# Kernel optimization log

Hardware: AMD Instinct MI355X
Metric: run time of the kernel (lower is better)

## Reference

```python
import jax, jax.numpy as jnp
import numpy as np

N, D = 10000, 20
NODE_DIM = 172
D_T = 172
EDGE_DIM = 172
N_HEAD = 2
D_MODEL = NODE_DIM + EDGE_DIM + D_T  # 516


def _layer_norm(x, g, b, eps=1e-5):
    mu = jnp.mean(x, axis=-1, keepdims=True)
    var = jnp.mean((x - mu) ** 2, axis=-1, keepdims=True)
    return (x - mu) / jnp.sqrt(var + eps) * g + b


def setup_inputs() -> dict:
    key = jax.random.key(0)
    ks = jax.random.split(key, 12)
    d_k = D_MODEL // N_HEAD
    std_qk = np.sqrt(2.0 / (D_MODEL + d_k)).astype(np.float32)
    node_h = jax.random.normal(ks[0], (N, NODE_DIM), jnp.float32)
    edge_t = jax.random.uniform(ks[1], (N, D), jnp.float32, 0.0, 100.0)
    edge_feat = jax.random.normal(ks[2], (N, D, EDGE_DIM), jnp.float32)
    nbr_idx = jax.random.randint(ks[3], (N, D), 0, N)
    t_now = jnp.array([100.0], jnp.float32)
    # weights stored [in, out]; apply as x @ W
    w_q = jax.random.normal(ks[4], (D_MODEL, N_HEAD * d_k), jnp.float32) * std_qk
    w_k = jax.random.normal(ks[5], (D_MODEL, N_HEAD * d_k), jnp.float32) * std_qk
    w_v = jax.random.normal(ks[6], (D_MODEL, N_HEAD * d_k), jnp.float32) * std_qk
    basis_freq = jnp.asarray(1.0 / 10 ** np.linspace(0, 9, D_T), jnp.float32)
    phase = jnp.zeros((D_T,), jnp.float32)
    ln_gamma = jnp.ones((D_MODEL,), jnp.float32)
    ln_beta = jnp.zeros((D_MODEL,), jnp.float32)
    fc_w = jax.random.normal(ks[7], (N_HEAD * d_k, D_MODEL), jnp.float32) * np.float32(np.sqrt(2.0 / (N_HEAD * d_k + D_MODEL)))
    fc_b = jnp.zeros((D_MODEL,), jnp.float32)
    m1_w = jax.random.normal(ks[8], (D_MODEL + NODE_DIM, NODE_DIM), jnp.float32) * np.float32(np.sqrt(2.0 / (D_MODEL + 2 * NODE_DIM)))
    m1_b = jnp.zeros((NODE_DIM,), jnp.float32)
    m2_w = jax.random.normal(ks[9], (NODE_DIM, NODE_DIM), jnp.float32) * np.float32(np.sqrt(1.0 / NODE_DIM))
    m2_b = jnp.zeros((NODE_DIM,), jnp.float32)
    return dict(node_h=node_h, edge_t=edge_t, edge_feat=edge_feat, nbr_idx=nbr_idx,
                t_now=t_now, n_head=N_HEAD, w_q=w_q, w_k=w_k, w_v=w_v,
                basis_freq=basis_freq, phase=phase, ln_gamma=ln_gamma, ln_beta=ln_beta,
                fc_w=fc_w, fc_b=fc_b, m1_w=m1_w, m1_b=m1_b, m2_w=m2_w, m2_b=m2_b)


def reference(node_h, edge_t, edge_feat, nbr_idx, t_now, n_head, w_q, w_k, w_v,
              basis_freq, phase, ln_gamma, ln_beta, fc_w, fc_b, m1_w, m1_b, m2_w, m2_b):
    n, deg = edge_t.shape
    d_model = w_q.shape[0]
    d_t = basis_freq.shape[0]
    edge_dim = d_model - node_h.shape[1] - d_t
    d_k = d_model // n_head
    # message_func: per-edge cosine time encoding + k/v projections
    t_enc = jnp.cos((t_now[0] - edge_t)[..., None] * basis_freq + phase)  # [N,D,d_T]
    z = jnp.concatenate([node_h[nbr_idx], edge_feat, t_enc], axis=-1)     # [N,D,d_model]
    k = z @ w_k                                                            # [N,D,H*dk]
    v = z @ w_v
    # reduce_func: self query (zero edge feat, cos(phase) time enc)
    self_z = jnp.concatenate([node_h,
                              jnp.zeros((n, edge_dim), node_h.dtype),
                              jnp.ones((n, d_t), node_h.dtype) * jnp.cos(phase)], axis=-1)
    q = self_z @ w_q                                                       # [N,H*dk]
    # reproduce the exact torch permute/view sequence (head-major flatten)
    qh = q.reshape(n, 1, n_head, d_k).transpose(2, 0, 1, 3).reshape(-1, 1, d_model)
    kh = k.reshape(n, deg, n_head, d_k).transpose(2, 0, 1, 3).reshape(-1, deg, d_model)
    vh = v.reshape(n, deg, n_head, d_k).transpose(2, 0, 1, 3).reshape(-1, deg, d_model)
    attn = jnp.einsum('bqd,bkd->bqk', qh, kh) / jnp.asarray(d_k ** 0.5, qh.dtype)
    attn = jax.nn.softmax(attn, axis=2)
    out = jnp.einsum('bqk,bkd->bqd', attn, vh)                             # [N,1,d_model]
    out = out[:, 0, :].reshape(n_head, n, d_k).transpose(1, 0, 2).reshape(n, -1)
    out = out @ fc_w + fc_b                                                # attn_fc (dropout in eval)
    h = _layer_norm(out + self_z, ln_gamma, ln_beta)
    # merger MLP
    x = jnp.concatenate([h, node_h], axis=-1)
    return jax.nn.relu(x @ m1_w + m1_b) @ m2_w + m2_b
```

## Files before the change

kernel.cpp:

```cpp
#include <hip/hip_runtime.h>
#include <hip/hip_bf16.h>
#include <math.h>

typedef __bf16 bf16;
typedef __attribute__((ext_vector_type(4))) __bf16 bf16x4;
typedef __attribute__((ext_vector_type(8))) __bf16 bf16x8;
typedef __attribute__((ext_vector_type(4))) float f32x4;

constexpr int NN   = 10000;
constexpr int NPAD = 10112;
constexpr int BM = 128, BN = 176, BK = 64;

constexpr size_t FCWT_OFF = 0;
constexpr size_t M1WT_OFF = 608256;
constexpr size_t M2WT_OFF = 856064;
constexpr size_t WKH_OFF  = 923648;
constexpr size_t WQHT_OFF = 1660928;
constexpr size_t WVH_OFF  = 2111488;
constexpr size_t WQKT_OFF = 3012608;
constexpr size_t WVFT_OFF = 3485696;
constexpr size_t QB_OFF   = 4702208;
constexpr size_t QKB_OFF  = 4706304;
constexpr size_t CPH_OFF  = 4714496;
constexpr size_t NH16_OFF = 4715520;
constexpr size_t QK_OFF   = NH16_OFF + (size_t)NPAD*192*2;
constexpr size_t ZB_OFF   = QK_OFF   + (size_t)NPAD*1152*2;
constexpr size_t FCR_OFF  = ZB_OFF   + (size_t)NPAD*1152*2;
constexpr size_t X_OFF    = FCR_OFF  + (size_t)NN*516*4;

typedef __attribute__((address_space(3))) void lds_void;
typedef const __attribute__((address_space(1))) void glb_void;
__device__ __forceinline__ void gload16(const void* g, void* l) {
    __builtin_amdgcn_global_load_lds((glb_void*)(uintptr_t)g,
                                     (lds_void*)(unsigned int)(uintptr_t)l, 16, 0, 0);
}

__global__ __launch_bounds__(256)
void packT_kernel(const float* __restrict__ fcw, const float* __restrict__ m1w,
                  const float* __restrict__ m2w,
                  bf16* __restrict__ FCWT, bf16* __restrict__ M1WT, bf16* __restrict__ M2WT) {
    __shared__ float tile[32][33];
    const float* src; bf16* dst; int K, C, LD;
    switch (blockIdx.y) {
        case 0:  src = fcw; K = 516; C = 516; dst = FCWT; LD = 576; break;
        case 1:  src = m1w; K = 688; C = 172; dst = M1WT; LD = 704; break;
        default: src = m2w; K = 172; C = 172; dst = M2WT; LD = 192; break;
    }
    const int tilesC = (C + 31) >> 5, tilesK = (K + 31) >> 5;
    const int nt = tilesC * tilesK;
    const int tx = threadIdx.x & 31, ty = threadIdx.x >> 5;
    for (int tb = blockIdx.x; tb < nt; tb += gridDim.x) {
        int tc = tb % tilesC, tk = tb / tilesC;
        #pragma unroll
        for (int i = 0; i < 4; ++i) {
            int k = tk*32 + ty + i*8, c = tc*32 + tx;
            tile[ty + i*8][tx] = (k < K && c < C) ? src[(size_t)k*C + c] : 0.f;
        }
        __syncthreads();
        #pragma unroll
        for (int i = 0; i < 4; ++i) {
            int c = tc*32 + ty + i*8, k = tk*32 + tx;
            if (c < C && k < K) dst[(size_t)c*LD + k] = (bf16)tile[tx][ty + i*8];
        }
        __syncthreads();
    }
}

__global__ void pack_misc_kernel(const float* __restrict__ wk, const float* __restrict__ wq,
                                 const float* __restrict__ wv, const float* __restrict__ node_h,
                                 const float* __restrict__ phase,
                                 bf16* __restrict__ WKH, bf16* __restrict__ WQHT,
                                 bf16* __restrict__ WVH, bf16* __restrict__ nh16,
                                 float* __restrict__ cph) {
    constexpr int T0 = 2*516*258;
    constexpr int T1 = T0 + 2*172*258;
    constexpr int T2 = T1 + 2*516*258;
    constexpr int T3 = T2 + NN*192;
    constexpr int T4 = T3 + 172;
    for (int idx = blockIdx.x * blockDim.x + threadIdx.x; idx < T4;
         idx += gridDim.x * blockDim.x) {
        if (idx < T0) {
            int h = idx / (516*258), rem = idx % (516*258), d = rem / 258, j = rem % 258;
            WKH[((size_t)h*576 + d)*320 + j] = (bf16)wk[(size_t)d*516 + h*258 + j];
        } else if (idx < T1) {
            int i = idx - T0;
            int h = i / (172*258), rem = i % (172*258), k = rem / 258, j = rem % 258;
            WQHT[((size_t)h*352 + k)*320 + j] = (bf16)wq[(size_t)k*516 + h*258 + j];
        } else if (idx < T2) {
            int i = idx - T1;
            int h = i / (516*258), rem = i % (516*258), c = rem / 258, j = rem % 258;
            WVH[((size_t)h*704 + c)*320 + j] = (bf16)wv[(size_t)c*516 + h*258 + j];
        } else if (idx < T3) {
            int i = idx - T2, r = i / 192, c = i % 192;
            nh16[i] = (c < 172) ? (bf16)node_h[(size_t)r*172 + c] : (bf16)0.f;
        } else cph[idx - T3] = cosf(phase[idx - T3]);
    }
}

__global__ __launch_bounds__(256)
void qbias_kernel(const float* __restrict__ w_q, const float* __restrict__ phase,
                  float* __restrict__ q_bias) {
    __shared__ float red[256];
    const int c = blockIdx.x, j = threadIdx.x;
    red[j] = (j < 172) ? cosf(phase[j]) * w_q[(size_t)(344 + j) * 516 + c] : 0.f;
    __syncthreads();
    #pragma unroll
    for (int o = 128; o; o >>= 1) { if (j < o) red[j] += red[j + o]; __syncthreads(); }
    if (j == 0) q_bias[c] = red[0];
}

__global__ __launch_bounds__(256)
void qkb_kernel(const float* __restrict__ wk, const float* __restrict__ QB,
                float* __restrict__ qkb) {
    __shared__ float red[256];
    const int hd = blockIdx.x, h = hd / 576, d = hd % 576, t = threadIdx.x;
    float a = 0.f;
    if (d < 516) {
        a = QB[h*258 + t] * wk[(size_t)d*516 + h*258 + t];
        if (t < 2) a += QB[h*258 + 256 + t] * wk[(size_t)d*516 + h*258 + 256 + t];
    }
    red[t] = a; __syncthreads();
    #pragma unroll
    for (int o = 128; o; o >>= 1) { if (t < o) red[t] += red[t + o]; __syncthreads(); }
    if (t == 0) qkb[hd] = red[0];
}

template<int KP, int EPI>
__global__ __launch_bounds__(256, 2)
void gemm_kernel(const bf16* __restrict__ A, int lda, const bf16* __restrict__ Bt,
                 float* __restrict__ outF, bf16* __restrict__ outB, int ldo,
                 const float* __restrict__ bias,
                 const float* __restrict__ aux0, const float* __restrict__ aux1,
                 int Mreal, int Nreal) {
    constexpr int NT = KP / BK;
    __shared__ __align__(16) bf16 As[2][BM][BK];
    __shared__ __align__(16) bf16 Bs[2][BN][BK];

    const int tid  = threadIdx.x;
    const int w    = tid >> 6;
    const int lane = tid & 63;
    const int lr   = lane & 15;
    const int ls   = lane >> 4;
    const int lrow = lane >> 3;
    const int lcol = (lane & 7) * 8;

    const bf16* aBase = A  + (size_t)(blockIdx.y * BM + w * 32 + lrow) * lda + lcol;
    const bf16* bBase = Bt + (size_t)(blockIdx.x * BN + lrow) * KP + lcol;

    auto stage = [&](int buf, int k0) {
        #pragma unroll
        for (int i = 0; i < 4; ++i)
            gload16(aBase + (size_t)(i * 8) * lda + k0, &As[buf][w * 32 + i * 8][0]);
        #pragma unroll
        for (int jj = 0; jj < 6; ++jj) {
            int j = jj * 4 + w;
            if (j < 22) gload16(bBase + (size_t)(j * 8) * KP + k0, &Bs[buf][j * 8][0]);
        }
    };

    f32x4 acc[2][11];
    #pragma unroll
    for (int a = 0; a < 2; ++a)
        #pragma unroll
        for (int b2 = 0; b2 < 11; ++b2) acc[a][b2] = (f32x4)(0.0f);

    stage(0, 0);
    __syncthreads();
    int cur = 0;
    for (int t = 0; t < NT; ++t) {
        if (t + 1 < NT) stage(cur ^ 1, (t + 1) * BK);
        #pragma unroll
        for (int kk = 0; kk < 2; ++kk) {
            bf16x8 a0 = *(const bf16x8*)&As[cur][w*32 +      lr][kk*32 + ls*8];
            bf16x8 a1 = *(const bf16x8*)&As[cur][w*32 + 16 + lr][kk*32 + ls*8];
            #pragma unroll
            for (int nt = 0; nt < 11; ++nt) {
                bf16x8 bfr = *(const bf16x8*)&Bs[cur][nt*16 + lr][kk*32 + ls*8];
                acc[0][nt] = __builtin_amdgcn_mfma_f32_16x16x32_bf16(a0, bfr, acc[0][nt], 0, 0, 0);
                acc[1][nt] = __builtin_amdgcn_mfma_f32_16x16x32_bf16(a1, bfr, acc[1][nt], 0, 0, 0);
            }
        }
        __syncthreads();
        cur ^= 1;
    }

    const int colb = blockIdx.x * BN + lr;
    const int rowb = blockIdx.y * BM + w*32 + ls*4;
    #pragma unroll
    for (int mt = 0; mt < 2; ++mt)
    #pragma unroll
    for (int nt = 0; nt < 11; ++nt)
    #pragma unroll
    for (int q2 = 0; q2 < 4; ++q2) {
        int row = rowb + mt*16 + q2;
        int col = colb + nt*16;
        if (row >= Mreal) continue;
        float v = acc[mt][nt][q2];
        if constexpr (EPI == 0) {
            if (col < Nreal) outB[(size_t)row*ldo + col] = (bf16)(v + bias[col]);
        } else {
            if (col < Nreal) {
                float sz = (col < 172) ? aux0[(size_t)row*172 + col]
                                       : ((col < 344) ? 0.f : aux1[col - 344]);
                outF[(size_t)row*ldo + col] = v + bias[col] + sz;
            }
        }
    }
}

__global__ __launch_bounds__(256, 2)
void gemm_multi_kernel(const bf16* __restrict__ WKH, const bf16* __restrict__ WQHT,
                       const bf16* __restrict__ FCWT, const bf16* __restrict__ WVH,
                       bf16* __restrict__ WQKT, bf16* __restrict__ WVFT) {
    constexpr int KP = 320, NT = KP / BK;
    const int z = blockIdx.z, h = z & 1;
    const bf16 *A, *Bt; bf16* outB; int lda, ldo, Mreal, Nreal;
    if (z < 2) {
        if (blockIdx.x >= 2) return;
        A = WKH + (size_t)h*576*320;  lda = 320;
        Bt = WQHT + (size_t)h*352*320;
        outB = WQKT + (size_t)h*576*192; ldo = 192; Mreal = 576; Nreal = 192;
    } else {
        A = FCWT + (size_t)h*258;     lda = 576;
        Bt = WVH + (size_t)h*704*320;
        outB = WVFT + (size_t)h*576;  ldo = 1152; Mreal = 516; Nreal = 576;
    }
    __shared__ __align__(16) bf16 As[2][BM][BK];
    __shared__ __align__(16) bf16 Bs[2][BN][BK];
    const int tid = threadIdx.x, w = tid >> 6, lane = tid & 63;
    const int lr = lane & 15, ls = lane >> 4;
    const int lrow = lane >> 3, lcol = (lane & 7) * 8;
    const bf16* aBase = A  + (size_t)(blockIdx.y * BM + w * 32 + lrow) * lda + lcol;
    const bf16* bBase = Bt + (size_t)(blockIdx.x * BN + lrow) * KP + lcol;
    auto stage = [&](int buf, int k0) {
        #pragma unroll
        for (int i = 0; i < 4; ++i)
            gload16(aBase + (size_t)(i * 8) * lda + k0, &As[buf][w * 32 + i * 8][0]);
        #pragma unroll
        for (int jj = 0; jj < 6; ++jj) {
            int j = jj * 4 + w;
            if (j < 22) gload16(bBase + (size_t)(j * 8) * KP + k0, &Bs[buf][j * 8][0]);
        }
    };
    f32x4 acc[2][11];
    #pragma unroll
    for (int a = 0; a < 2; ++a)
        #pragma unroll
        for (int b2 = 0; b2 < 11; ++b2) acc[a][b2] = (f32x4)(0.0f);
    stage(0, 0);
    __syncthreads();
    int cur = 0;
    for (int t = 0; t < NT; ++t) {
        if (t + 1 < NT) stage(cur ^ 1, (t + 1) * BK);
        #pragma unroll
        for (int kk = 0; kk < 2; ++kk) {
            bf16x8 a0 = *(const bf16x8*)&As[cur][w*32 +      lr][kk*32 + ls*8];
            bf16x8 a1 = *(const bf16x8*)&As[cur][w*32 + 16 + lr][kk*32 + ls*8];
            #pragma unroll
            for (int nt = 0; nt < 11; ++nt) {
                bf16x8 bfr = *(const bf16x8*)&Bs[cur][nt*16 + lr][kk*32 + ls*8];
                acc[0][nt] = __builtin_amdgcn_mfma_f32_16x16x32_bf16(a0, bfr, acc[0][nt], 0, 0, 0);
                acc[1][nt] = __builtin_amdgcn_mfma_f32_16x16x32_bf16(a1, bfr, acc[1][nt], 0, 0, 0);
            }
        }
        __syncthreads();
        cur ^= 1;
    }
    const int colb = blockIdx.x * BN + lr;
    const int rowb = blockIdx.y * BM + w*32 + ls*4;
    #pragma unroll
    for (int mt = 0; mt < 2; ++mt)
    #pragma unroll
    for (int nt = 0; nt < 11; ++nt)
    #pragma unroll
    for (int q2 = 0; q2 < 4; ++q2) {
        int row = rowb + mt*16 + q2;
        int col = colb + nt*16;
        if (row < Mreal && col < Nreal)
            outB[(size_t)row*ldo + col] = (bf16)acc[mt][nt][q2];
    }
}

__global__ __launch_bounds__(256, 3)
void attn_lite_kernel(const bf16* __restrict__ QK, const bf16* __restrict__ nh16,
                      const float* __restrict__ edge_feat, const float* __restrict__ edge_t,
                      const int* __restrict__ nbr_idx, const float* __restrict__ freq,
                      const float* __restrict__ ph, const float* __restrict__ tnow,
                      bf16* __restrict__ ZB) {
    __shared__ __align__(16) bf16 zs[40 * 576];
    __shared__ __align__(16) float G[40][4];
    __shared__ float sfreq[172], sph[172];
    __shared__ float sdt[40];
    __shared__ int   ssrc[40];
    __shared__ float pp[2][20];

    const int r  = blockIdx.x;
    const int iA = 2 * r;
    const int t  = threadIdx.x;
    const int w  = t >> 6, lane = t & 63;
    const int lr = lane & 15, ls = lane >> 4;

    auto zsa = [&](int row, int c) -> bf16* {
        unsigned b = (unsigned)(row * 1152 + c * 2) ^ (unsigned)((row & 7) << 4);
        return (bf16*)((char*)zs + b);
    };

    f32x4 efA[4], efB[4];
    #pragma unroll
    for (int s = 0; s < 4; ++s) {
        int idx = t + (s + 3) * 256;
        if (idx >= 880 && idx < 1720) {
            int i2 = idx - 880;
            int row = i2 / 21, c = 22 + i2 % 21;
            const float* ep = edge_feat + (size_t)(iA * 20 + row) * 172 + (c * 8 - 172);
            efA[s] = *(const f32x4*)ep;
            efB[s] = *(const f32x4*)(ep + 4);
        }
    }

    if (t < 172) { sfreq[t] = freq[t]; sph[t] = ph[t]; }
    if (t >= 192 && t < 232) {
        int e2 = t - 192, ge = iA * 20 + e2;
        sdt[e2]  = tnow[0] - edge_t[ge];
        ssrc[e2] = nbr_idx[ge];
    }
    __syncthreads();

    #pragma unroll
    for (int it = 0; it < 4; ++it) {
        int idx = t + it * 256;
        if (idx < 880) {
            int row = idx / 22, c = idx % 22;
            bf16x8 v;
            if (c < 21) {
                v = *(const bf16x8*)(nh16 + (size_t)ssrc[row] * 192 + c * 8);
            } else {
                int ge = iA * 20 + row;
                #pragma unroll
                for (int e = 0; e < 8; ++e) {
                    int k = 168 + e;
                    v[e] = (k < 172) ? nh16[(size_t)ssrc[row] * 192 + k]
                                     : (bf16)edge_feat[(size_t)ge * 172 + (k - 172)];
                }
            }
            *(bf16x8*)zsa(row, c * 8) = v;
        }
    }
    #pragma unroll
    for (int it = 6; it < 12; ++it) {
        int idx = t + it * 256;
        if (idx >= 1720 && idx < 2880) {
            int row, c;
            bf16x8 v;
            if (idx < 2600) {
                int i3 = idx - 1720;
                row = i3 / 22; c = 43 + i3 % 22;
                float dt = sdt[row];
                int k0 = c * 8;
                #pragma unroll
                for (int e = 0; e < 8; ++e) {
                    int k = k0 + e;
                    v[e] = (k < 516) ? (bf16)__cosf(dt * sfreq[k - 344] + sph[k - 344]) : (bf16)0.f;
                }
            } else {
                int i4 = idx - 2600;
                row = i4 / 7; c = 65 + i4 % 7;
                #pragma unroll
                for (int e = 0; e < 8; ++e) v[e] = (bf16)0.f;
            }
            *(bf16x8*)zsa(row, c * 8) = v;
        }
    }
    #pragma unroll
    for (int s = 0; s < 4; ++s) {
        int idx = t + (s + 3) * 256;
        if (idx >= 880 && idx < 1720) {
            int i2 = idx - 880;
            int row = i2 / 21, c = 22 + i2 % 21;
            bf16x8 v;
            #pragma unroll
            for (int e = 0; e < 4; ++e) { v[e] = (bf16)efA[s][e]; v[e+4] = (bf16)efB[s][e]; }
            *(bf16x8*)zsa(row, c * 8) = v;
        }
    }
    __syncthreads();

    if (w < 3) {
        int brow = w * 16 + lr; if (brow > 39) brow = 39;
        const bf16* aQK = QK + (size_t)(iA + ((lr >> 1) & 1)) * 1152 + (lane & 1) * 576;
        f32x4 acc = (f32x4)(0.0f);
        __builtin_amdgcn_s_setprio(1);
        #pragma unroll
        for (int ks = 0; ks < 18; ++ks) {
            bf16x8 af = *(const bf16x8*)(aQK + ks * 32 + ls * 8);
            bf16x8 bf = *(const bf16x8*)zsa(brow, ks * 32 + ls * 8);
            acc = __builtin_amdgcn_mfma_f32_16x16x32_bf16(af, bf, acc, 0, 0, 0);
        }
        __builtin_amdgcn_s_setprio(0);
        int col = w * 16 + lr;
        if (ls == 0 && col < 40) *(f32x4*)&G[col][0] = acc;
    }
    __syncthreads();

    if (t < 64) {
        int h = lane >> 5, knbr = lane & 31;
        bool act = knbr < 20;
        float l = -1e30f;
        if (act) {
            int z0 = (knbr / 10) * 20 + 2 * (knbr % 10);
            l = (G[z0][h] + G[z0 + 1][2 + h]) * 0.0622573006f;
        }
        float m = l;
        #pragma unroll
        for (int o = 16; o >= 1; o >>= 1) m = fmaxf(m, __shfl_xor(m, o));
        float e = act ? __expf(l - m) : 0.f;
        float s2 = e;
        #pragma unroll
        for (int o = 16; o >= 1; o >>= 1) s2 += __shfl_xor(s2, o);
        if (act) pp[h][knbr] = e / s2;
    }
    __syncthreads();

    #pragma unroll
    for (int it = 0; it < 2; ++it) {
        int idx = t + it * 256;
        if (idx < 288) {
            int nsel = idx / 144, c4 = (idx % 144) * 4;
            float a0[4] = {0.f, 0.f, 0.f, 0.f};
            float a1[4] = {0.f, 0.f, 0.f, 0.f};
            #pragma unroll
            for (int knbr = 0; knbr < 20; ++knbr) {
                int z0 = (knbr / 10) * 20 + 2 * (knbr % 10) + nsel;
                bf16x4 zv = *(const bf16x4*)zsa(z0, c4);
                float p0 = pp[0][knbr], p1 = pp[1][knbr];
                #pragma unroll
                for (int i = 0; i < 4; ++i) {
                    float zf = (float)zv[i];
                    a0[i] += p0 * zf;
                    a1[i] += p1 * zf;
                }
            }
            bf16x4 o0, o1;
            #pragma unroll
            for (int i = 0; i < 4; ++i) { o0[i] = (bf16)a0[i]; o1[i] = (bf16)a1[i]; }
            *(bf16x4*)(ZB + (size_t)(iA + nsel) * 1152 + c4)       = o0;
            *(bf16x4*)(ZB + (size_t)(iA + nsel) * 1152 + 576 + c4) = o1;
        }
    }
}

__global__ __launch_bounds__(256)
void ln_x_kernel(const float* __restrict__ fcr, const float* __restrict__ g,
                 const float* __restrict__ b, const bf16* __restrict__ nh16,
                 bf16* __restrict__ X) {
    __shared__ float red[2][4];
    __shared__ float mb[2];
    const size_t i = blockIdx.x;
    const int t = threadIdx.x;
    int c0 = t, c1 = t + 256, c2 = t + 512;
    float v0 = fcr[i*516 + c0];
    float v1 = (c1 < 516) ? fcr[i*516 + c1] : 0.f;
    float v2 = (c2 < 516) ? fcr[i*516 + c2] : 0.f;
    float s = v0 + v1 + v2, ss = v0*v0 + v1*v1 + v2*v2;
    #pragma unroll
    for (int o = 32; o; o >>= 1) { s += __shfl_down(s, o); ss += __shfl_down(ss, o); }
    if ((t & 63) == 0) { red[0][t >> 6] = s; red[1][t >> 6] = ss; }
    __syncthreads();
    if (t == 0) {
        float S  = red[0][0] + red[0][1] + red[0][2] + red[0][3];
        float SS = red[1][0] + red[1][1] + red[1][2] + red[1][3];
        float mean = S / 516.f;
        float var  = SS / 516.f - mean*mean;
        mb[0] = mean; mb[1] = rsqrtf(var + 1e-5f);
    }
    __syncthreads();
    float mean = mb[0], rstd = mb[1];
    X[i*704 + c0] = (bf16)((v0 - mean)*rstd*g[c0] + b[c0]);
    if (c1 < 516) X[i*704 + c1] = (bf16)((v1 - mean)*rstd*g[c1] + b[c1]);
    if (c2 < 516) X[i*704 + c2] = (bf16)((v2 - mean)*rstd*g[c2] + b[c2]);
    for (int c = 516 + t; c < 704; c += 256)
        X[i*704 + c] = (c < 688) ? nh16[i*192 + (c - 516)] : (bf16)0.f;
}

__global__ __launch_bounds__(256)
void m1m2_kernel(const bf16* __restrict__ A, const bf16* __restrict__ B1,
                 const bf16* __restrict__ B2, const float* __restrict__ b1,
                 const float* __restrict__ b2, float* __restrict__ outF, int Mreal) {
    constexpr int KP = 704, NT = KP / BK;
    __shared__ __align__(16) union {
        struct { bf16 As[2][BM][BK]; bf16 Bs[2][BN][BK]; } g;
        struct { bf16 Rs[BM][192];  bf16 B2s[BN][192]; } s;
    } U;

    const int tid  = threadIdx.x;
    const int w    = tid >> 6;
    const int lane = tid & 63;
    const int lr   = lane & 15;
    const int ls   = lane >> 4;
    const int lrow = lane >> 3;
    const int lcol = (lane & 7) * 8;

    const bf16* aBase = A  + (size_t)(blockIdx.y * BM + w * 32 + lrow) * KP + lcol;
    const bf16* bBase = B1 + (size_t)lrow * KP + lcol;

    auto stage = [&](int buf, int k0) {
        #pragma unroll
        for (int i = 0; i < 4; ++i)
            gload16(aBase + (size_t)(i * 8) * KP + k0, &U.g.As[buf][w * 32 + i * 8][0]);
        #pragma unroll
        for (int jj = 0; jj < 6; ++jj) {
            int j = jj * 4 + w;
            if (j < 22) gload16(bBase + (size_t)(j * 8) * KP + k0, &U.g.Bs[buf][j * 8][0]);
        }
    };

    f32x4 acc[2][11];
    #pragma unroll
    for (int a = 0; a < 2; ++a)
        #pragma unroll
        for (int b = 0; b < 11; ++b) acc[a][b] = (f32x4)(0.0f);

    stage(0, 0);
    __syncthreads();
    int cur = 0;
    for (int t = 0; t < NT; ++t) {
        if (t + 1 < NT) stage(cur ^ 1, (t + 1) * BK);
        #pragma unroll
        for (int kk = 0; kk < 2; ++kk) {
            bf16x8 a0 = *(const bf16x8*)&U.g.As[cur][w*32 +      lr][kk*32 + ls*8];
            bf16x8 a1 = *(const bf16x8*)&U.g.As[cur][w*32 + 16 + lr][kk*32 + ls*8];
            #pragma unroll
            for (int nt = 0; nt < 11; ++nt) {
                bf16x8 bfr = *(const bf16x8*)&U.g.Bs[cur][nt*16 + lr][kk*32 + ls*8];
                acc[0][nt] = __builtin_amdgcn_mfma_f32_16x16x32_bf16(a0, bfr, acc[0][nt], 0, 0, 0);
                acc[1][nt] = __builtin_amdgcn_mfma_f32_16x16x32_bf16(a1, bfr, acc[1][nt], 0, 0, 0);
            }
        }
        __syncthreads();
        cur ^= 1;
    }

    #pragma unroll
    for (int mt = 0; mt < 2; ++mt)
    #pragma unroll
    for (int nt = 0; nt < 11; ++nt)
    #pragma unroll
    for (int q2 = 0; q2 < 4; ++q2) {
        int lro = w*32 + mt*16 + ls*4 + q2;
        int col = lr + nt*16;
        float vv = (col < 172) ? fmaxf(acc[mt][nt][q2] + b1[col], 0.f) : 0.f;
        U.s.Rs[lro][col] = (bf16)vv;
    }
    for (int idx = tid; idx < BM*16; idx += 256)
        U.s.Rs[idx >> 4][176 + (idx & 15)] = (bf16)0.f;
    #pragma unroll
    for (int jj = 0; jj < 17; ++jj) {
        int j = jj * 4 + w;
        if (j < 66)
            gload16(B2 + (size_t)j*512 + lane*8, (bf16*)U.s.B2s + (size_t)j*512 + lane*8);
    }
    __syncthreads();

    f32x4 acc2[2][11];
    #pragma unroll
    for (int a = 0; a < 2; ++a)
        #pragma unroll
        for (int b = 0; b < 11; ++b) acc2[a][b] = (f32x4)(0.0f);
    #pragma unroll
    for (int t2 = 0; t2 < 3; ++t2) {
        #pragma unroll
        for (int kk = 0; kk < 2; ++kk) {
            int off = t2*64 + kk*32 + ls*8;
            bf16x8 a0 = *(const bf16x8*)&U.s.Rs[w*32 +      lr][off];
            bf16x8 a1 = *(const bf16x8*)&U.s.Rs[w*32 + 16 + lr][off];
            #pragma unroll
            for (int nt = 0; nt < 11; ++nt) {
                bf16x8 bfr = *(const bf16x8*)&U.s.B2s[nt*16 + lr][off];
                acc2[0][nt] = __builtin_amdgcn_mfma_f32_16x16x32_bf16(a0, bfr, acc2[0][nt], 0, 0, 0);
                acc2[1][nt] = __builtin_amdgcn_mfma_f32_16x16x32_bf16(a1, bfr, acc2[1][nt], 0, 0, 0);
            }
        }
    }

    const int rowb = blockIdx.y * BM + w*32 + ls*4;
    #pragma unroll
    for (int mt = 0; mt < 2; ++mt)
    #pragma unroll
    for (int nt = 0; nt < 11; ++nt)
    #pragma unroll
    for (int q2 = 0; q2 < 4; ++q2) {
        int row = rowb + mt*16 + q2;
        int col = lr + nt*16;
        if (row < Mreal && col < 172)
            outF[(size_t)row*172 + col] = acc2[mt][nt][q2] + b2[col];
    }
}

extern "C" void kernel_launch(void* const* d_in, const int* in_sizes, int n_in,
                              void* d_out, int out_size, void* d_ws, size_t ws_size,
                              hipStream_t stream) {
    const float* node_h     = (const float*)d_in[0];
    const float* edge_t     = (const float*)d_in[1];
    const float* edge_feat  = (const float*)d_in[2];
    const int*   nbr_idx    = (const int*)d_in[3];
    const float* t_now      = (const float*)d_in[4];
    const float* w_q        = (const float*)d_in[6];
    const float* w_k        = (const float*)d_in[7];
    const float* w_v        = (const float*)d_in[8];
    const float* basis_freq = (const float*)d_in[9];
    const float* phase      = (const float*)d_in[10];
    const float* ln_g       = (const float*)d_in[11];
    const float* ln_b       = (const float*)d_in[12];
    const float* fc_w       = (const float*)d_in[13];
    const float* fc_b       = (const float*)d_in[14];
    const float* m1_w       = (const float*)d_in[15];
    const float* m1_b       = (const float*)d_in[16];
    const float* m2_w       = (const float*)d_in[17];
    const float* m2_b       = (const float*)d_in[18];

    char* ws = (char*)d_ws;
    bf16*  FCWT = (bf16*)(ws + FCWT_OFF);
    bf16*  M1WT = (bf16*)(ws + M1WT_OFF);
    bf16*  M2WT = (bf16*)(ws + M2WT_OFF);
    bf16*  WKH  = (bf16*)(ws + WKH_OFF);
    bf16*  WQHT = (bf16*)(ws + WQHT_OFF);
    bf16*  WVH  = (bf16*)(ws + WVH_OFF);
    bf16*  WQKT = (bf16*)(ws + WQKT_OFF);
    bf16*  WVFT = (bf16*)(ws + WVFT_OFF);
    float* QB   = (float*)(ws + QB_OFF);
    float* QKB  = (float*)(ws + QKB_OFF);
    float* CPH  = (float*)(ws + CPH_OFF);
    bf16*  NH16 = (bf16*)(ws + NH16_OFF);
    bf16*  QK   = (bf16*)(ws + QK_OFF);
    bf16*  ZB   = (bf16*)(ws + ZB_OFF);
    float* FCR  = (float*)(ws + FCR_OFF);
    bf16*  Xb   = (bf16*)(ws + X_OFF);

    hipMemsetAsync(ws, 0, NH16_OFF, stream);

    packT_kernel<<<dim3(289, 3), 256, 0, stream>>>(fc_w, m1_w, m2_w, FCWT, M1WT, M2WT);
    pack_misc_kernel<<<2048, 256, 0, stream>>>(w_k, w_q, w_v, node_h, phase,
                                               WKH, WQHT, WVH, NH16, CPH);
    qbias_kernel<<<516, 256, 0, stream>>>(w_q, phase, QB);
    qkb_kernel<<<1152, 256, 0, stream>>>(w_k, QB, QKB);

    gemm_multi_kernel<<<dim3(4, 5, 4), 256, 0, stream>>>(WKH, WQHT, FCWT, WVH, WQKT, WVFT);

    gemm_kernel<192, 0><<<dim3(7, 79), 256, 0, stream>>>(
        NH16, 192, WQKT, nullptr, QK, 1152, QKB, nullptr, nullptr, NN, 1152);

    attn_lite_kernel<<<NN / 2, 256, 0, stream>>>(
        QK, NH16, edge_feat, edge_t, nbr_idx, basis_freq, phase, t_now, ZB);

    gemm_kernel<1152, 2><<<dim3(3, 79), 256, 0, stream>>>(
        ZB, 1152, WVFT, FCR, nullptr, 516, fc_b, node_h, CPH, NN, 516);

    ln_x_kernel<<<NN, 256, 0, stream>>>(FCR, ln_g, ln_b, NH16, Xb);

    m1m2_kernel<<<dim3(1, 79), 256, 0, stream>>>(
        Xb, M1WT, M2WT, m1_b, m2_b, (float*)d_out, NN);
}
```

Before: 263.8 us.

## Process two node pairs per attention block with register-staged prefetch overlap

The attention kernel now handles two node pairs per block and launches half as many blocks. While the first pair's scores, softmax and weighted sum are computed, the second pair's gathered neighbor features and edge features are loaded from global memory into registers. The edge-feature boundary chunk is now read with vector loads instead of per-element scalar loads. This aims to hide gather latency behind compute, at the cost of more registers and extra barriers, which may lower occupancy.

```diff
diff --git a/kernel.cpp b/kernel.cpp
--- a/kernel.cpp
+++ b/kernel.cpp
@@ -290,163 +290,185 @@
     __shared__ __align__(16) bf16 zs[40 * 576];
     __shared__ __align__(16) float G[40][4];
     __shared__ float sfreq[172], sph[172];
-    __shared__ float sdt[40];
-    __shared__ int   ssrc[40];
+    __shared__ float sdt[2][40];
+    __shared__ int   ssrc[2][40];
     __shared__ float pp[2][20];
 
-    const int r  = blockIdx.x;
-    const int iA = 2 * r;
-    const int t  = threadIdx.x;
-    const int w  = t >> 6, lane = t & 63;
-    const int lr = lane & 15, ls = lane >> 4;
+    const int t    = threadIdx.x;
+    const int w    = t >> 6, lane = t & 63;
+    const int lr   = lane & 15, ls = lane >> 4;
+    const int rp0  = blockIdx.x * 2;
 
     auto zsa = [&](int row, int c) -> bf16* {
         unsigned b = (unsigned)(row * 1152 + c * 2) ^ (unsigned)((row & 7) << 4);
         return (bf16*)((char*)zs + b);
     };
 
-    f32x4 efA[4], efB[4];
-    #pragma unroll
-    for (int s = 0; s < 4; ++s) {
-        int idx = t + (s + 3) * 256;
-        if (idx >= 880 && idx < 1720) {
-            int i2 = idx - 880;
-            int row = i2 / 21, c = 22 + i2 % 21;
-            const float* ep = edge_feat + (size_t)(iA * 20 + row) * 172 + (c * 8 - 172);
-            efA[s] = *(const f32x4*)ep;
-            efB[s] = *(const f32x4*)(ep + 4);
-        }
-    }
-
     if (t < 172) { sfreq[t] = freq[t]; sph[t] = ph[t]; }
-    if (t >= 192 && t < 232) {
-        int e2 = t - 192, ge = iA * 20 + e2;
-        sdt[e2]  = tnow[0] - edge_t[ge];
-        ssrc[e2] = nbr_idx[ge];
-    }
-    __syncthreads();
-
-    #pragma unroll
-    for (int it = 0; it < 4; ++it) {
-        int idx = t + it * 256;
-        if (idx < 880) {
-            int row = idx / 22, c = idx % 22;
-            bf16x8 v;
-            if (c < 21) {
-                v = *(const bf16x8*)(nh16 + (size_t)ssrc[row] * 192 + c * 8);
-            } else {
-                int ge = iA * 20 + row;
+    if (t >= 176) {
+        int e2 = t - 176;
+        int ge = rp0 * 40 + e2;
+        sdt[e2 / 40][e2 % 40]  = tnow[0] - edge_t[ge];
+        ssrc[e2 / 40][e2 % 40] = nbr_idx[ge];
+    }
+    __syncthreads();
+
+    bf16x8 nhA[4]; bf16x4 nhm[4]; f32x4 efm[4]; f32x4 efA[4], efB[4];
+
+    auto STAGE = [&](int p) {
+        const int base = (rp0 + p) * 40;
+        #pragma unroll
+        for (int s = 0; s < 4; ++s) {
+            int i = t + s * 256;
+            if (i < 880) {
+                int row = i / 22, c = i % 22;
+                if (c < 21) {
+                    nhA[s] = *(const bf16x8*)(nh16 + (size_t)ssrc[p][row] * 192 + c * 8);
+                } else {
+                    nhm[s] = *(const bf16x4*)(nh16 + (size_t)ssrc[p][row] * 192 + 168);
+                    efm[s] = *(const f32x4*)(edge_feat + (size_t)(base + row) * 172);
+                }
+            }
+        }
+        #pragma unroll
+        for (int s = 0; s < 4; ++s) {
+            int i2 = t + s * 256;
+            if (i2 < 840) {
+                int row = i2 / 21, c = 22 + i2 % 21;
+                const float* ep = edge_feat + (size_t)(base + row) * 172 + (c * 8 - 172);
+                efA[s] = *(const f32x4*)ep;
+                efB[s] = *(const f32x4*)(ep + 4);
+            }
+        }
+    };
+
+    auto WRITE = [&](int p) {
+        #pragma unroll
+        for (int s = 0; s < 4; ++s) {
+            int i = t + s * 256;
+            if (i < 880) {
+                int row = i / 22, c = i % 22;
+                if (c < 21) {
+                    *(bf16x8*)zsa(row, c * 8) = nhA[s];
+                } else {
+                    bf16x8 v;
+                    v[0] = nhm[s][0]; v[1] = nhm[s][1]; v[2] = nhm[s][2]; v[3] = nhm[s][3];
+                    v[4] = (bf16)efm[s][0]; v[5] = (bf16)efm[s][1];
+                    v[6] = (bf16)efm[s][2]; v[7] = (bf16)efm[s][3];
+                    *(bf16x8*)zsa(row, 168) = v;
+                }
+            }
+        }
+        #pragma unroll
+        for (int s = 0; s < 4; ++s) {
+            int i2 = t + s * 256;
+            if (i2 < 840) {
+                int row = i2 / 21, c = 22 + i2 % 21;
+                bf16x8 v;
                 #pragma unroll
-                for (int e = 0; e < 8; ++e) {
-                    int k = 168 + e;
-                    v[e] = (k < 172) ? nh16[(size_t)ssrc[row] * 192 + k]
-                                     : (bf16)edge_feat[(size_t)ge * 172 + (k - 172)];
+                for (int e = 0; e < 4; ++e) { v[e] = (bf16)efA[s][e]; v[e+4] = (bf16)efB[s][e]; }
+                *(bf16x8*)zsa(row, c * 8) = v;
+            }
+        }
+        #pragma unroll
+        for (int it = 6; it < 12; ++it) {
+            int idx = t + it * 256;
+            if (idx >= 1720 && idx < 2880) {
+                int row, c; bf16x8 v;
+                if (idx < 2600) {
+                    int i3 = idx - 1720;
+                    row = i3 / 22; c = 43 + i3 % 22;
+                    float dt = sdt[p][row];
+                    int k0 = c * 8;
+                    #pragma unroll
+                    for (int e = 0; e < 8; ++e) {
+                        int k = k0 + e;
+                        v[e] = (k < 516) ? (bf16)__cosf(dt * sfreq[k - 344] + sph[k - 344]) : (bf16)0.f;
+                    }
+                } else {
+                    int i4 = idx - 2600;
+                    row = i4 / 7; c = 65 + i4 % 7;
+                    #pragma unroll
+                    for (int e = 0; e < 8; ++e) v[e] = (bf16)0.f;
                 }
-            }
-            *(bf16x8*)zsa(row, c * 8) = v;
-        }
-    }
-    #pragma unroll
-    for (int it = 6; it < 12; ++it) {
-        int idx = t + it * 256;
-        if (idx >= 1720 && idx < 2880) {
-            int row, c;
-            bf16x8 v;
-            if (idx < 2600) {
-                int i3 = idx - 1720;
-                row = i3 / 22; c = 43 + i3 % 22;
-                float dt = sdt[row];
-                int k0 = c * 8;
+                *(bf16x8*)zsa(row, c * 8) = v;
+            }
+        }
+    };
+
+    auto COMPUTE = [&](int p) {
+        const int iA = (rp0 + p) * 2;
+        if (w < 3) {
+            int brow = w * 16 + lr; if (brow > 39) brow = 39;
+            const bf16* aQK = QK + (size_t)(iA + ((lr >> 1) & 1)) * 1152 + (lane & 1) * 576;
+            f32x4 acc = (f32x4)(0.0f);
+            __builtin_amdgcn_s_setprio(1);
+            #pragma unroll
+            for (int ks = 0; ks < 18; ++ks) {
+                bf16x8 af = *(const bf16x8*)(aQK + ks * 32 + ls * 8);
+                bf16x8 bf = *(const bf16x8*)zsa(brow, ks * 32 + ls * 8);
+                acc = __builtin_amdgcn_mfma_f32_16x16x32_bf16(af, bf, acc, 0, 0, 0);
+            }
+            __builtin_amdgcn_s_setprio(0);
+            int col = w * 16 + lr;
+            if (ls == 0 && col < 40) *(f32x4*)&G[col][0] = acc;
+        }
+        __syncthreads();
+        if (t < 64) {
+            int h = lane >> 5, knbr = lane & 31;
+            bool act = knbr < 20;
+            float l = -1e30f;
+            if (act) {
+                int z0 = (knbr / 10) * 20 + 2 * (knbr % 10);
+                l = (G[z0][h] + G[z0 + 1][2 + h]) * 0.0622573006f;
+            }
+            float m = l;
+            #pragma unroll
+            for (int o = 16; o >= 1; o >>= 1) m = fmaxf(m, __shfl_xor(m, o));
+            float e = act ? __expf(l - m) : 0.f;
+            float s2 = e;
+            #pragma unroll
+            for (int o = 16; o >= 1; o >>= 1) s2 += __shfl_xor(s2, o);
+            if (act) pp[h][knbr] = e / s2;
+        }
+        __syncthreads();
+        #pragma unroll
+        for (int it = 0; it < 2; ++it) {
+            int idx = t + it * 256;
+            if (idx < 288) {
+                int nsel = idx / 144, c4 = (idx % 144) * 4;
+                float a0[4] = {0.f, 0.f, 0.f, 0.f};
+                float a1[4] = {0.f, 0.f, 0.f, 0.f};
                 #pragma unroll
-                for (int e = 0; e < 8; ++e) {
-                    int k = k0 + e;
-                    v[e] = (k < 516) ? (bf16)__cosf(dt * sfreq[k - 344] + sph[k - 344]) : (bf16)0.f;
+                for (int knbr = 0; knbr < 20; ++knbr) {
+                    int z0 = (knbr / 10) * 20 + 2 * (knbr % 10) + nsel;
+                    bf16x4 zv = *(const bf16x4*)zsa(z0, c4);
+                    float p0 = pp[0][knbr], p1 = pp[1][knbr];
+                    #pragma unroll
+                    for (int i = 0; i < 4; ++i) {
+                        float zf = (float)zv[i];
+                        a0[i] += p0 * zf;
+                        a1[i] += p1 * zf;
+                    }
                 }
-            } else {
-                int i4 = idx - 2600;
-                row = i4 / 7; c = 65 + i4 % 7;
+                bf16x4 o0, o1;
                 #pragma unroll
-                for (int e = 0; e < 8; ++e) v[e] = (bf16)0.f;
-            }
-            *(bf16x8*)zsa(row, c * 8) = v;
-        }
-    }
-    #pragma unroll
-    for (int s = 0; s < 4; ++s) {
-        int idx = t + (s + 3) * 256;
-        if (idx >= 880 && idx < 1720) {
-            int i2 = idx - 880;
-            int row = i2 / 21, c = 22 + i2 % 21;
-            bf16x8 v;
-            #pragma unroll
-            for (int e = 0; e < 4; ++e) { v[e] = (bf16)efA[s][e]; v[e+4] = (bf16)efB[s][e]; }
-            *(bf16x8*)zsa(row, c * 8) = v;
-        }
-    }
-    __syncthreads();
-
-    if (w < 3) {
-        int brow = w * 16 + lr; if (brow > 39) brow = 39;
-        const bf16* aQK = QK + (size_t)(iA + ((lr >> 1) & 1)) * 1152 + (lane & 1) * 576;
-        f32x4 acc = (f32x4)(0.0f);
-        __builtin_amdgcn_s_setprio(1);
-        #pragma unroll
-        for (int ks = 0; ks < 18; ++ks) {
-            bf16x8 af = *(const bf16x8*)(aQK + ks * 32 + ls * 8);
-            bf16x8 bf = *(const bf16x8*)zsa(brow, ks * 32 + ls * 8);
-            acc = __builtin_amdgcn_mfma_f32_16x16x32_bf16(af, bf, acc, 0, 0, 0);
-        }
-        __builtin_amdgcn_s_setprio(0);
-        int col = w * 16 + lr;
-        if (ls == 0 && col < 40) *(f32x4*)&G[col][0] = acc;
-    }
-    __syncthreads();
-
-    if (t < 64) {
-        int h = lane >> 5, knbr = lane & 31;
-        bool act = knbr < 20;
-        float l = -1e30f;
-        if (act) {
-            int z0 = (knbr / 10) * 20 + 2 * (knbr % 10);
-            l = (G[z0][h] + G[z0 + 1][2 + h]) * 0.0622573006f;
-        }
-        float m = l;
-        #pragma unroll
-        for (int o = 16; o >= 1; o >>= 1) m = fmaxf(m, __shfl_xor(m, o));
-        float e = act ? __expf(l - m) : 0.f;
-        float s2 = e;
-        #pragma unroll
-        for (int o = 16; o >= 1; o >>= 1) s2 += __shfl_xor(s2, o);
-        if (act) pp[h][knbr] = e / s2;
-    }
-    __syncthreads();
-
-    #pragma unroll
-    for (int it = 0; it < 2; ++it) {
-        int idx = t + it * 256;
-        if (idx < 288) {
-            int nsel = idx / 144, c4 = (idx % 144) * 4;
-            float a0[4] = {0.f, 0.f, 0.f, 0.f};
-            float a1[4] = {0.f, 0.f, 0.f, 0.f};
-            #pragma unroll
-            for (int knbr = 0; knbr < 20; ++knbr) {
-                int z0 = (knbr / 10) * 20 + 2 * (knbr % 10) + nsel;
-                bf16x4 zv = *(const bf16x4*)zsa(z0, c4);
-                float p0 = pp[0][knbr], p1 = pp[1][knbr];
-                #pragma unroll
-                for (int i = 0; i < 4; ++i) {
-                    float zf = (float)zv[i];
-                    a0[i] += p0 * zf;
-                    a1[i] += p1 * zf;
-                }
-            }
-            bf16x4 o0, o1;
-            #pragma unroll
-            for (int i = 0; i < 4; ++i) { o0[i] = (bf16)a0[i]; o1[i] = (bf16)a1[i]; }
-            *(bf16x4*)(ZB + (size_t)(iA + nsel) * 1152 + c4)       = o0;
-            *(bf16x4*)(ZB + (size_t)(iA + nsel) * 1152 + 576 + c4) = o1;
-        }
-    }
+                for (int i = 0; i < 4; ++i) { o0[i] = (bf16)a0[i]; o1[i] = (bf16)a1[i]; }
+                *(bf16x4*)(ZB + (size_t)(iA + nsel) * 1152 + c4)       = o0;
+                *(bf16x4*)(ZB + (size_t)(iA + nsel) * 1152 + 576 + c4) = o1;
+            }
+        }
+    };
+
+    STAGE(0);
+    WRITE(0);
+    __syncthreads();
+    STAGE(1);
+    COMPUTE(0);
+    __syncthreads();
+    WRITE(1);
+    __syncthreads();
+    COMPUTE(1);
 }
 
 __global__ __launch_bounds__(256)
@@ -649,7 +671,7 @@
     gemm_kernel<192, 0><<<dim3(7, 79), 256, 0, stream>>>(
         NH16, 192, WQKT, nullptr, QK, 1152, QKB, nullptr, nullptr, NN, 1152);
 
-    attn_lite_kernel<<<NN / 2, 256, 0, stream>>>(
+    attn_lite_kernel<<<NN / 4, 256, 0, stream>>>(
         QK, NH16, edge_feat, edge_t, nbr_idx, basis_freq, phase, t_now, ZB);
 
     gemm_kernel<1152, 2><<<dim3(3, 79), 256, 0, stream>>>(
```

New measurement: 273.3 us. 3.6% more time.

## Halve GEMM M-tile to 64 rows and split fused m1m2 into two GEMMs

Applied to the files above, without the earlier changes.

Parameterizes the generic GEMM on M-tile size and launches all main GEMMs with 64-row tiles, doubling the grid to fill more CUs on the 10000-row problems. The fused m1/m2 MLP kernel, which ran only 79 blocks, is replaced by two launches of the generic GEMM (ReLU+bf16 epilogue, then bias epilogue) with an intermediate buffer in workspace. This trades extra B-tile reloads per block and an extra global round-trip plus launch for much higher parallelism.

```diff
diff --git a/kernel.cpp b/kernel.cpp
--- a/kernel.cpp
+++ b/kernel.cpp
@@ -9,7 +9,7 @@
 
 constexpr int NN   = 10000;
 constexpr int NPAD = 10112;
-constexpr int BM = 128, BN = 176, BK = 64;
+constexpr int BN = 176, BK = 64;
 
 constexpr size_t FCWT_OFF = 0;
 constexpr size_t M1WT_OFF = 608256;
@@ -27,6 +27,7 @@
 constexpr size_t ZB_OFF   = QK_OFF   + (size_t)NPAD*1152*2;
 constexpr size_t FCR_OFF  = ZB_OFF   + (size_t)NPAD*1152*2;
 constexpr size_t X_OFF    = FCR_OFF  + (size_t)NN*516*4;
+constexpr size_t R_OFF    = X_OFF    + (size_t)NPAD*704*2;
 
 typedef __attribute__((address_space(3))) void lds_void;
 typedef const __attribute__((address_space(1))) void glb_void;
@@ -125,15 +126,16 @@
     if (t == 0) qkb[hd] = red[0];
 }
 
-template<int KP, int EPI>
+template<int KP, int EPI, int MT>
 __global__ __launch_bounds__(256, 2)
 void gemm_kernel(const bf16* __restrict__ A, int lda, const bf16* __restrict__ Bt,
                  float* __restrict__ outF, bf16* __restrict__ outB, int ldo,
                  const float* __restrict__ bias,
                  const float* __restrict__ aux0, const float* __restrict__ aux1,
                  int Mreal, int Nreal) {
-    constexpr int NT = KP / BK;
-    __shared__ __align__(16) bf16 As[2][BM][BK];
+    constexpr int NT  = KP / BK;
+    constexpr int BMt = 64 * MT;
+    __shared__ __align__(16) bf16 As[2][BMt][BK];
     __shared__ __align__(16) bf16 Bs[2][BN][BK];
 
     const int tid  = threadIdx.x;
@@ -144,13 +146,13 @@
     const int lrow = lane >> 3;
     const int lcol = (lane & 7) * 8;
 
-    const bf16* aBase = A  + (size_t)(blockIdx.y * BM + w * 32 + lrow) * lda + lcol;
+    const bf16* aBase = A  + (size_t)(blockIdx.y * BMt + w * 16 * MT + lrow) * lda + lcol;
     const bf16* bBase = Bt + (size_t)(blockIdx.x * BN + lrow) * KP + lcol;
 
     auto stage = [&](int buf, int k0) {
         #pragma unroll
-        for (int i = 0; i < 4; ++i)
-            gload16(aBase + (size_t)(i * 8) * lda + k0, &As[buf][w * 32 + i * 8][0]);
+        for (int i = 0; i < 2 * MT; ++i)
+            gload16(aBase + (size_t)(i * 8) * lda + k0, &As[buf][w * 16 * MT + i * 8][0]);
         #pragma unroll
         for (int jj = 0; jj < 6; ++jj) {
             int j = jj * 4 + w;
@@ -158,9 +160,9 @@
         }
     };
 
-    f32x4 acc[2][11];
-    #pragma unroll
-    for (int a = 0; a < 2; ++a)
+    f32x4 acc[MT][11];
+    #pragma unroll
+    for (int a = 0; a < MT; ++a)
         #pragma unroll
         for (int b2 = 0; b2 < 11; ++b2) acc[a][b2] = (f32x4)(0.0f);
 
@@ -171,13 +173,16 @@
         if (t + 1 < NT) stage(cur ^ 1, (t + 1) * BK);
         #pragma unroll
         for (int kk = 0; kk < 2; ++kk) {
-            bf16x8 a0 = *(const bf16x8*)&As[cur][w*32 +      lr][kk*32 + ls*8];
-            bf16x8 a1 = *(const bf16x8*)&As[cur][w*32 + 16 + lr][kk*32 + ls*8];
+            bf16x8 afr[MT];
+            #pragma unroll
+            for (int mt = 0; mt < MT; ++mt)
+                afr[mt] = *(const bf16x8*)&As[cur][w*16*MT + mt*16 + lr][kk*32 + ls*8];
             #pragma unroll
             for (int nt = 0; nt < 11; ++nt) {
                 bf16x8 bfr = *(const bf16x8*)&Bs[cur][nt*16 + lr][kk*32 + ls*8];
-                acc[0][nt] = __builtin_amdgcn_mfma_f32_16x16x32_bf16(a0, bfr, acc[0][nt], 0, 0, 0);
-                acc[1][nt] = __builtin_amdgcn_mfma_f32_16x16x32_bf16(a1, bfr, acc[1][nt], 0, 0, 0);
+                #pragma unroll
+                for (int mt = 0; mt < MT; ++mt)
+                    acc[mt][nt] = __builtin_amdgcn_mfma_f32_16x16x32_bf16(afr[mt], bfr, acc[mt][nt], 0, 0, 0);
             }
         }
         __syncthreads();
@@ -185,9 +190,9 @@
     }
 
     const int colb = blockIdx.x * BN + lr;
-    const int rowb = blockIdx.y * BM + w*32 + ls*4;
-    #pragma unroll
-    for (int mt = 0; mt < 2; ++mt)
+    const int rowb = blockIdx.y * BMt + w*16*MT + ls*4;
+    #pragma unroll
+    for (int mt = 0; mt < MT; ++mt)
     #pragma unroll
     for (int nt = 0; nt < 11; ++nt)
     #pragma unroll
@@ -198,12 +203,17 @@
         float v = acc[mt][nt][q2];
         if constexpr (EPI == 0) {
             if (col < Nreal) outB[(size_t)row*ldo + col] = (bf16)(v + bias[col]);
-        } else {
+        } else if constexpr (EPI == 2) {
             if (col < Nreal) {
                 float sz = (col < 172) ? aux0[(size_t)row*172 + col]
                                        : ((col < 344) ? 0.f : aux1[col - 344]);
                 outF[(size_t)row*ldo + col] = v + bias[col] + sz;
             }
+        } else if constexpr (EPI == 3) {
+            float vv = (col < Nreal) ? fmaxf(v + bias[col], 0.f) : 0.f;
+            outB[(size_t)row*ldo + col] = (bf16)vv;
+        } else {
+            if (col < Nreal) outF[(size_t)row*ldo + col] = v + bias[col];
         }
     }
 }
@@ -225,12 +235,12 @@
         Bt = WVH + (size_t)h*704*320;
         outB = WVFT + (size_t)h*576;  ldo = 1152; Mreal = 516; Nreal = 576;
     }
-    __shared__ __align__(16) bf16 As[2][BM][BK];
+    __shared__ __align__(16) bf16 As[2][128][BK];
     __shared__ __align__(16) bf16 Bs[2][BN][BK];
     const int tid = threadIdx.x, w = tid >> 6, lane = tid & 63;
     const int lr = lane & 15, ls = lane >> 4;
     const int lrow = lane >> 3, lcol = (lane & 7) * 8;
-    const bf16* aBase = A  + (size_t)(blockIdx.y * BM + w * 32 + lrow) * lda + lcol;
+    const bf16* aBase = A  + (size_t)(blockIdx.y * 128 + w * 32 + lrow) * lda + lcol;
     const bf16* bBase = Bt + (size_t)(blockIdx.x * BN + lrow) * KP + lcol;
     auto stage = [&](int buf, int k0) {
         #pragma unroll
@@ -267,7 +277,7 @@
         cur ^= 1;
     }
     const int colb = blockIdx.x * BN + lr;
-    const int rowb = blockIdx.y * BM + w*32 + ls*4;
+    const int rowb = blockIdx.y * 128 + w*32 + ls*4;
     #pragma unroll
     for (int mt = 0; mt < 2; ++mt)
     #pragma unroll
@@ -482,120 +492,6 @@
         X[i*704 + c] = (c < 688) ? nh16[i*192 + (c - 516)] : (bf16)0.f;
 }
 
-__global__ __launch_bounds__(256)
-void m1m2_kernel(const bf16* __restrict__ A, const bf16* __restrict__ B1,
-                 const bf16* __restrict__ B2, const float* __restrict__ b1,
-                 const float* __restrict__ b2, float* __restrict__ outF, int Mreal) {
-    constexpr int KP = 704, NT = KP / BK;
-    __shared__ __align__(16) union {
-        struct { bf16 As[2][BM][BK]; bf16 Bs[2][BN][BK]; } g;
-        struct { bf16 Rs[BM][192];  bf16 B2s[BN][192]; } s;
-    } U;
-
-    const int tid  = threadIdx.x;
-    const int w    = tid >> 6;
-    const int lane = tid & 63;
-    const int lr   = lane & 15;
-    const int ls   = lane >> 4;
-    const int lrow = lane >> 3;
-    const int lcol = (lane & 7) * 8;
-
-    const bf16* aBase = A  + (size_t)(blockIdx.y * BM + w * 32 + lrow) * KP + lcol;
-    const bf16* bBase = B1 + (size_t)lrow * KP + lcol;
-
-    auto stage = [&](int buf, int k0) {
-        #pragma unroll
-        for (int i = 0; i < 4; ++i)
-            gload16(aBase + (size_t)(i * 8) * KP + k0, &U.g.As[buf][w * 32 + i * 8][0]);
-        #pragma unroll
-        for (int jj = 0; jj < 6; ++jj) {
-            int j = jj * 4 + w;
-            if (j < 22) gload16(bBase + (size_t)(j * 8) * KP + k0, &U.g.Bs[buf][j * 8][0]);
-        }
-    };
-
-    f32x4 acc[2][11];
-    #pragma unroll
-    for (int a = 0; a < 2; ++a)
-        #pragma unroll
-        for (int b = 0; b < 11; ++b) acc[a][b] = (f32x4)(0.0f);
-
-    stage(0, 0);
-    __syncthreads();
-    int cur = 0;
-    for (int t = 0; t < NT; ++t) {
-        if (t + 1 < NT) stage(cur ^ 1, (t + 1) * BK);
-        #pragma unroll
-        for (int kk = 0; kk < 2; ++kk) {
-            bf16x8 a0 = *(const bf16x8*)&U.g.As[cur][w*32 +      lr][kk*32 + ls*8];
-            bf16x8 a1 = *(const bf16x8*)&U.g.As[cur][w*32 + 16 + lr][kk*32 + ls*8];
-            #pragma unroll
-            for (int nt = 0; nt < 11; ++nt) {
-                bf16x8 bfr = *(const bf16x8*)&U.g.Bs[cur][nt*16 + lr][kk*32 + ls*8];
-                acc[0][nt] = __builtin_amdgcn_mfma_f32_16x16x32_bf16(a0, bfr, acc[0][nt], 0, 0, 0);
-                acc[1][nt] = __builtin_amdgcn_mfma_f32_16x16x32_bf16(a1, bfr, acc[1][nt], 0, 0, 0);
-            }
-        }
-        __syncthreads();
-        cur ^= 1;
-    }
-
-    #pragma unroll
-    for (int mt = 0; mt < 2; ++mt)
-    #pragma unroll
-    for (int nt = 0; nt < 11; ++nt)
-    #pragma unroll
-    for (int q2 = 0; q2 < 4; ++q2) {
-        int lro = w*32 + mt*16 + ls*4 + q2;
-        int col = lr + nt*16;
-        float vv = (col < 172) ? fmaxf(acc[mt][nt][q2] + b1[col], 0.f) : 0.f;
-        U.s.Rs[lro][col] = (bf16)vv;
-    }
-    for (int idx = tid; idx < BM*16; idx += 256)
-        U.s.Rs[idx >> 4][176 + (idx & 15)] = (bf16)0.f;
-    #pragma unroll
-    for (int jj = 0; jj < 17; ++jj) {
-        int j = jj * 4 + w;
-        if (j < 66)
-            gload16(B2 + (size_t)j*512 + lane*8, (bf16*)U.s.B2s + (size_t)j*512 + lane*8);
-    }
-    __syncthreads();
-
-    f32x4 acc2[2][11];
-    #pragma unroll
-    for (int a = 0; a < 2; ++a)
-        #pragma unroll
-        for (int b = 0; b < 11; ++b) acc2[a][b] = (f32x4)(0.0f);
-    #pragma unroll
-    for (int t2 = 0; t2 < 3; ++t2) {
-        #pragma unroll
-        for (int kk = 0; kk < 2; ++kk) {
-            int off = t2*64 + kk*32 + ls*8;
-            bf16x8 a0 = *(const bf16x8*)&U.s.Rs[w*32 +      lr][off];
-            bf16x8 a1 = *(const bf16x8*)&U.s.Rs[w*32 + 16 + lr][off];
-            #pragma unroll
-            for (int nt = 0; nt < 11; ++nt) {
-                bf16x8 bfr = *(const bf16x8*)&U.s.B2s[nt*16 + lr][off];
-                acc2[0][nt] = __builtin_amdgcn_mfma_f32_16x16x32_bf16(a0, bfr, acc2[0][nt], 0, 0, 0);
-                acc2[1][nt] = __builtin_amdgcn_mfma_f32_16x16x32_bf16(a1, bfr, acc2[1][nt], 0, 0, 0);
-            }
-        }
-    }
-
-    const int rowb = blockIdx.y * BM + w*32 + ls*4;
-    #pragma unroll
-    for (int mt = 0; mt < 2; ++mt)
-    #pragma unroll
-    for (int nt = 0; nt < 11; ++nt)
-    #pragma unroll
-    for (int q2 = 0; q2 < 4; ++q2) {
-        int row = rowb + mt*16 + q2;
-        int col = lr + nt*16;
-        if (row < Mreal && col < 172)
-            outF[(size_t)row*172 + col] = acc2[mt][nt][q2] + b2[col];
-    }
-}
-
 extern "C" void kernel_launch(void* const* d_in, const int* in_sizes, int n_in,
                               void* d_out, int out_size, void* d_ws, size_t ws_size,
                               hipStream_t stream) {
@@ -635,6 +531,7 @@
     bf16*  ZB   = (bf16*)(ws + ZB_OFF);
     float* FCR  = (float*)(ws + FCR_OFF);
     bf16*  Xb   = (bf16*)(ws + X_OFF);
+    bf16*  Rb   = (bf16*)(ws + R_OFF);
 
     hipMemsetAsync(ws, 0, NH16_OFF, stream);
 
@@ -646,17 +543,20 @@
 
     gemm_multi_kernel<<<dim3(4, 5, 4), 256, 0, stream>>>(WKH, WQHT, FCWT, WVH, WQKT, WVFT);
 
-    gemm_kernel<192, 0><<<dim3(7, 79), 256, 0, stream>>>(
+    gemm_kernel<192, 0, 1><<<dim3(7, 158), 256, 0, stream>>>(
         NH16, 192, WQKT, nullptr, QK, 1152, QKB, nullptr, nullptr, NN, 1152);
 
     attn_lite_kernel<<<NN / 2, 256, 0, stream>>>(
         QK, NH16, edge_feat, edge_t, nbr_idx, basis_freq, phase, t_now, ZB);
 
-    gemm_kernel<1152, 2><<<dim3(3, 79), 256, 0, stream>>>(
+    gemm_kernel<1152, 2, 1><<<dim3(3, 158), 256, 0, stream>>>(
         ZB, 1152, WVFT, FCR, nullptr, 516, fc_b, node_h, CPH, NN, 516);
 
     ln_x_kernel<<<NN, 256, 0, stream>>>(FCR, ln_g, ln_b, NH16, Xb);
 
-    m1m2_kernel<<<dim3(1, 79), 256, 0, stream>>>(
-        Xb, M1WT, M2WT, m1_b, m2_b, (float*)d_out, NN);
-}
+    gemm_kernel<704, 3, 1><<<dim3(1, 158), 256, 0, stream>>>(
+        Xb, 704, M1WT, nullptr, Rb, 192, m1_b, nullptr, nullptr, NN, 172);
+
+    gemm_kernel<192, 4, 1><<<dim3(1, 158), 256, 0, stream>>>(
+        Rb, 192, M2WT, (float*)d_out, nullptr, 172, m2_b, nullptr, nullptr, NN, 172);
+}
```

New measurement: 251.0 us. 4.9% less time.
